# Performance work log

Hardware: AMD Instinct MI355X
Metric: run time of the kernel (lower is better)

## Reference

```python
import jax, jax.numpy as jnp
import numpy as np
import math

EPS = 1e-8
ROUTING_ITERS = 2
FINAL_LAMBDA = 0.01

B, O, I, D_IN, D_OUT = 64, 64, 1152, 16, 16


def setup_inputs() -> dict:
    key = jax.random.key(0)
    k1, k2, k3, k4, k5 = jax.random.split(key, 5)
    stdev = 0.2
    u = jax.random.normal(k1, (B, I, D_IN), dtype=jnp.float32)
    W = jax.random.normal(k2, (1, O, I, D_OUT, D_IN), dtype=jnp.float32) * stdev
    beta_a = jax.random.normal(k3, (1, O), dtype=jnp.float32) * stdev
    beta_u = jax.random.normal(k4, (1, O, 1, 1), dtype=jnp.float32) * stdev
    bias = jnp.full((1, O, D_OUT), 0.1, dtype=jnp.float32)
    return {"u": u, "W": W, "beta_a": beta_a, "beta_u": beta_u, "bias": bias}


def _m_step(rr, V, a_i, beta_a, beta_u, inv_temp):
    # rr: (B,O,I), V: (B,O,I,D), a_i: (B,I)
    rra = rr * a_i[:, None, :]                      # (B,O,I)
    rr_sum = jnp.sum(rra, axis=-1, keepdims=True)   # (B,O,1)
    mean_j = jnp.sum(rra[..., None] * V, axis=2) / (rr_sum + EPS)       # (B,O,D)
    diff = V - mean_j[:, :, None, :]
    var_j = jnp.sum(rra[..., None] * diff * diff, axis=2) / (rr_sum + EPS) + 1e-4  # (B,O,D)
    # beta_u broadcast: original stores (1,O,1) tiled over out_dim
    cost_j = jnp.sum((beta_u[..., 0] + jnp.log(var_j)) * rr_sum, axis=-1)  # (B,O)
    a_j = jax.nn.sigmoid(inv_temp * (beta_a - cost_j))                     # (B,O)
    return mean_j, var_j, a_j


def _e_step(mean_j, var_j, a_j, V):
    diff = V - mean_j[:, :, None, :]                                  # (B,O,I,D)
    p1 = jnp.sqrt(2.0 * math.pi * jnp.prod(var_j, axis=-1) + EPS)     # (B,O)
    log_arg = -jnp.sum(diff * diff / (2.0 * var_j[:, :, None, :] + EPS), axis=-1)  # (B,O,I)
    p_ij = jnp.exp(log_arg) / (p1[:, :, None] + EPS)                  # (B,O,I)
    ap = a_j[:, :, None] * p_ij
    rr = ap / (jnp.sum(ap, axis=1, keepdims=True) + EPS)
    return rr


def reference(u, W, beta_a, beta_u, bias):
    # votes: V[b,o,i,e] = sum_d u[b,i,d] * W[0,o,i,e,d]
    a_i = jnp.linalg.norm(u + EPS, axis=-1)                           # (B,I)
    V = jnp.einsum('bid,oied->boie', u, W[0]) + EPS + bias[:, :, None, :]  # (B,O,I,D)
    batch = u.shape[0]
    out_caps = W.shape[1]
    rr = jnp.full((batch, out_caps, V.shape[2]), 1.0 / out_caps, dtype=u.dtype)
    for i in range(ROUTING_ITERS):
        inv_temp = FINAL_LAMBDA * (1.0 - 0.95 ** (i + 1))
        mean_j, var_j, a_j = _m_step(rr, V, a_i, beta_a, beta_u, inv_temp)
        if i < ROUTING_ITERS - 1:
            rr = _e_step(mean_j, var_j, a_j, V)
    out = a_j[:, :, None] * mean_j / (jnp.linalg.norm(mean_j + EPS, axis=-1, keepdims=True) + EPS)
    return out
```

## Files before the change

kernel.cpp:

```cpp
#include <hip/hip_runtime.h>

#define EPSF 1e-8f

constexpr int NB = 64;
constexpr int NO = 64;
constexpr int NI = 1152;
constexpr int ND = 16;

constexpr int RSTRIDE = 260;
constexpr int BUFSZ   = 64 * RSTRIDE;

typedef float v2f __attribute__((ext_vector_type(2)));
typedef float v4f __attribute__((ext_vector_type(4)));


__device__ __forceinline__ void loadrow16f(const float* __restrict__ base,
                                           size_t elem, float* f){
  const float4* p = (const float4*)(base + elem);
  float4 x0=p[0], x1=p[1], x2=p[2], x3=p[3];
  f[0]=x0.x; f[1]=x0.y; f[2]=x0.z; f[3]=x0.w;
  f[4]=x1.x; f[5]=x1.y; f[6]=x1.z; f[7]=x1.w;
  f[8]=x2.x; f[9]=x2.y; f[10]=x2.z; f[11]=x2.w;
  f[12]=x3.x; f[13]=x3.y; f[14]=x3.z; f[15]=x3.w;
}

__device__ __forceinline__ void gl_lds16(const float* g, float* l){
  __builtin_amdgcn_global_load_lds(
      (const __attribute__((address_space(1))) unsigned int*)g,
      (__attribute__((address_space(3))) unsigned int*)l,
      16, 0, 0);
}

__global__ __launch_bounds__(256, 2) void k_mpass(
    const float* __restrict__ u, const float* __restrict__ W,
    float* __restrict__ S1p, float* __restrict__ S2p, float* __restrict__ Wsp,
    const int CH)
{
  const int CI = NI / CH;
  const int bid = blockIdx.x;
  const int bg = bid / CH, c = bid % CH;
  const int t = threadIdx.x, lane = t & 63, w = t >> 6;
  const int b0 = bg*8 + 2*w, b1 = b0 + 1;
  const int i0 = c*CI;

  __shared__ float buf[BUFSZ];

  v2f S1[16], S2[16]; v2f wsum = {0.f, 0.f};
  #pragma unroll
  for (int e=0;e<16;++e){ S1[e]=v2f{0.f,0.f}; S2[e]=v2f{0.f,0.f}; }

  const float* row = &buf[lane*RSTRIDE];

  for (int ii=0; ii<CI; ++ii){
    const int i = i0 + ii;
    __syncthreads();
    {
      const float* g = W + (size_t)i*256 + (size_t)(w*16)*NI*256
                         + (size_t)lane*4;
      float* l = buf + (w*16)*RSTRIDE;
      #pragma unroll 1
      for (int r=0;r<16;++r){
        gl_lds16(g, l);
        g += (size_t)NI*256;
        l += RSTRIDE;
      }
    }

    v2f u01[16];
    {
      const float4* pa = (const float4*)(u + ((size_t)b0*NI + i)*ND);
      const float4* pb = (const float4*)(u + ((size_t)b1*NI + i)*ND);
      #pragma unroll
      for (int q=0;q<4;++q){
        float4 xa = pa[q], xb = pb[q];
        u01[q*4+0] = v2f{xa.x, xb.x};
        u01[q*4+1] = v2f{xa.y, xb.y};
        u01[q*4+2] = v2f{xa.z, xb.z};
        u01[q*4+3] = v2f{xa.w, xb.w};
      }
    }
    v2f ss = {0.f, 0.f};
    #pragma unroll
    for (int d=0;d<16;++d){ v2f x = u01[d] + EPSF; ss += x*x; }
    const v2f av = {sqrtf(ss.x), sqrtf(ss.y)};

    __syncthreads();

    #pragma unroll
    for (int e=0;e<16;++e){
      v2f Ve = {0.f, 0.f};
      #pragma unroll
      for (int dq=0; dq<4; ++dq){
        const float4 wv = *(const float4*)(row + e*16 + dq*4);
        const int d = dq*4;
        Ve += wv.x*u01[d+0];
        Ve += wv.y*u01[d+1];
        Ve += wv.z*u01[d+2];
        Ve += wv.w*u01[d+3];
      }
      v2f tv = av*Ve;
      S1[e] += tv;
      S2[e] += tv*Ve;
    }
    wsum += av;
  }

  const size_t ba = (((size_t)b0*CH + c)*NO + lane);
  const size_t bb = (((size_t)b1*CH + c)*NO + lane);
  #pragma unroll
  for (int e=0;e<16;++e){
    S1p[ba*ND+e]=S1[e].x; S2p[ba*ND+e]=S2[e].x;
    S1p[bb*ND+e]=S1[e].y; S2p[bb*ND+e]=S2[e].y;
  }
  Wsp[ba] = wsum.x; Wsp[bb] = wsum.y;
}

template<int NW, bool ESTEP>
__global__ __launch_bounds__(NW*64, 2) void k_heavy(
    const float* __restrict__ u, const float* __restrict__ W,
    const float* __restrict__ bias,
    const float* __restrict__ mean0, const float* __restrict__ i2v0,
    const float* __restrict__ c0,
    float* __restrict__ S1p, float* __restrict__ S2p, float* __restrict__ Wsp,
    const int CH)
{
  const int CI = NI / CH;
  constexpr int ROWS = 64 / NW;
  const int bid = blockIdx.x;
  const int bg = bid / CH, c = bid % CH;
  const int t = threadIdx.x, lane = t & 63, w = t >> 6;
  const int b0 = bg*(2*NW) + 2*w, b1 = b0 + 1;
  const int i0 = c*CI;

  __shared__ float buf[2*BUFSZ];

  float bs[16]; loadrow16f(bias, (size_t)lane*ND, bs);
  v2f mr[16], ir[16]; v2f c01 = {0.f, 0.f};
  if (ESTEP){
    const size_t m0 = ((size_t)b0*NO + lane)*ND;
    const size_t m1 = ((size_t)b1*NO + lane)*ND;
    #pragma unroll
    for (int e=0;e<16;++e){
      mr[e] = v2f{mean0[m0+e], mean0[m1+e]};
      ir[e] = v2f{i2v0[m0+e], i2v0[m1+e]};
    }
    c01 = v2f{c0[(size_t)b0*NO + lane], c0[(size_t)b1*NO + lane]};
  }

  v2f S1[16], S2[16]; v2f wsum = {0.f, 0.f};
  #pragma unroll
  for (int e=0;e<16;++e){ S1[e]=v2f{0.f,0.f}; S2[e]=v2f{0.f,0.f}; }

  auto stage = [&](int p, int i){
    const float* gbase = W + (size_t)i*256 + (size_t)lane*4;
    float* lbase = &buf[p*BUFSZ];
    #pragma unroll
    for (int r=0;r<ROWS;++r){
      const int o = w*ROWS + r;
      gl_lds16(gbase + (size_t)o*NI*256, lbase + o*RSTRIDE);
    }
  };

  int p = 0;
  stage(0, i0);

  for (int ii=0; ii<CI; ++ii){
    __syncthreads();
    if (ii+1 < CI) stage(p^1, i0+ii+1);

    const int i = i0 + ii;
    v2f u01[16];
    {
      const float4* pa = (const float4*)(u + ((size_t)b0*NI + i)*ND);
      const float4* pb = (const float4*)(u + ((size_t)b1*NI + i)*ND);
      #pragma unroll
      for (int q=0;q<4;++q){
        float4 xa = pa[q], xb = pb[q];
        u01[q*4+0] = v2f{xa.x, xb.x};
        u01[q*4+1] = v2f{xa.y, xb.y};
        u01[q*4+2] = v2f{xa.z, xb.z};
        u01[q*4+3] = v2f{xa.w, xb.w};
      }
    }
    v2f ss = {0.f, 0.f};
    #pragma unroll
    for (int d=0;d<16;++d){ v2f x = u01[d] + EPSF; ss += x*x; }
    const v2f av = {sqrtf(ss.x), sqrtf(ss.y)};

    v2f V[16];
    #pragma unroll
    for (int e=0;e<16;++e){ float b = bs[e] + EPSF; V[e] = v2f{b, b}; }
    const float* row = &buf[p*BUFSZ + lane*RSTRIDE];
    #pragma unroll
    for (int e=0;e<16;++e){
      #pragma unroll
      for (int dq=0; dq<4; ++dq){
        const float4 wv = *(const float4*)(row + e*16 + dq*4);
        const int d = dq*4;
        V[e] += wv.x*u01[d+0];
        V[e] += wv.y*u01[d+1];
        V[e] += wv.z*u01[d+2];
        V[e] += wv.w*u01[d+3];
      }
    }

    v2f wg;
    if (ESTEP){
      v2f la = {0.f, 0.f};
      #pragma unroll
      for (int e=0;e<16;++e){ v2f df = V[e]-mr[e]; la += df*df*ir[e]; }
      v2f ap = c01 * v2f{__expf(-la.x), __expf(-la.y)};
      float q0 = ap.x, q1 = ap.y;
      #pragma unroll
      for (int off=32; off; off>>=1){
        q0 += __shfl_xor(q0, off);
        q1 += __shfl_xor(q1, off);
      }
      wg = v2f{ap.x/(q0 + EPSF)*av.x, ap.y/(q1 + EPSF)*av.y};
    } else {
      wg = av;
    }
    wsum += wg;
    #pragma unroll
    for (int e=0;e<16;++e){
      v2f tv = wg*V[e]; S1[e]+=tv; S2[e]+=tv*V[e];
    }
    p ^= 1;
  }

  const size_t ba = (((size_t)b0*CH + c)*NO + lane);
  const size_t bb = (((size_t)b1*CH + c)*NO + lane);
  #pragma unroll
  for (int e=0;e<16;++e){
    S1p[ba*ND+e]=S1[e].x; S2p[ba*ND+e]=S2[e].x;
    S1p[bb*ND+e]=S1[e].y; S2p[bb*ND+e]=S2[e].y;
  }
  Wsp[ba] = wsum.x; Wsp[bb] = wsum.y;
}

__global__ __launch_bounds__(64) void k_mred(
    const float* __restrict__ beta_a, const float* __restrict__ beta_u,
    const float* __restrict__ bias,
    const float* __restrict__ S1p, const float* __restrict__ S2p,
    const float* __restrict__ Wsp, const int CH,
    float* __restrict__ mean0, float* __restrict__ i2v0, float* __restrict__ c0)
{
  const int bo = blockIdx.x;
  const int b = bo >> 6, o = bo & 63;
  const int t = threadIdx.x;
  const int q = t & 3, cg = t >> 2;

  v4f s1 = {0.f,0.f,0.f,0.f}, s2 = {0.f,0.f,0.f,0.f};
  for (int c = cg; c < CH; c += 16){
    const size_t base = ((((size_t)b*CH)+c)*NO + o)*ND + 4*q;
    s1 += *(const v4f*)(S1p + base);
    s2 += *(const v4f*)(S2p + base);
  }
  #pragma unroll
  for (int off=4; off<64; off<<=1){
    #pragma unroll
    for (int k=0;k<4;++k){
      s1[k] += __shfl_xor(s1[k], off);
      s2[k] += __shfl_xor(s2[k], off);
    }
  }
  float wv = 0.f;
  for (int c = t; c < CH; c += 64)
    wv += Wsp[(((size_t)b*CH)+c)*NO + o];
  #pragma unroll
  for (int off=1; off<64; off<<=1) wv += __shfl_xor(wv, off);

  {
    v4f Bq = *(const v4f*)(bias + (size_t)o*ND + 4*q);
    Bq += EPSF;
    s2 += 2.f*Bq*s1 + Bq*Bq*wv;
    s1 += Bq*wv;
  }

  const float rrsum = wv * (1.f/64.f);
  const float inv = 1.f/(rrsum + EPSF);
  const float bu = beta_u[o];
  v4f T1 = s1*(1.f/64.f), T2 = s2*(1.f/64.f);
  v4f m   = T1*inv;
  v4f var = (T2 - 2.f*m*T1 + m*m*rrsum)*inv + 1e-4f;
  v4f iv;
  float ctp = 0.f, prp = 1.f;
  #pragma unroll
  for (int k=0;k<4;++k){
    iv[k] = 1.f/(2.f*var[k] + EPSF);
    ctp += bu + __logf(var[k]);
    prp *= var[k];
  }
  ctp += __shfl_xor(ctp, 1); ctp += __shfl_xor(ctp, 2);
  prp *= __shfl_xor(prp, 1); prp *= __shfl_xor(prp, 2);

  const size_t mbase = ((size_t)b*NO + o)*ND;
  if (cg == 0){
    *(v4f*)(mean0 + mbase + 4*q) = m;
    *(v4f*)(i2v0  + mbase + 4*q) = iv;
  }
  if (t == 0){
    float cost = ctp * rrsum;
    float x  = 5.0e-4f*(beta_a[o] - cost);
    float aj = 1.f/(1.f + __expf(-x));
    float p1 = sqrtf(6.2831853071795864f*prp + EPSF);
    c0[(size_t)b*NO + o] = aj/(p1 + EPSF);
  }
}

__global__ __launch_bounds__(64) void k_final(
    const float* __restrict__ beta_a, const float* __restrict__ beta_u,
    const float* __restrict__ S1p, const float* __restrict__ S2p,
    const float* __restrict__ Wsp, const int CH,
    float* __restrict__ out)
{
  const int bo = blockIdx.x;
  const int b = bo >> 6, o = bo & 63;
  const int t = threadIdx.x;
  const int q = t & 3, cg = t >> 2;

  v4f s1 = {0.f,0.f,0.f,0.f}, s2 = {0.f,0.f,0.f,0.f};
  for (int c = cg; c < CH; c += 16){
    const size_t base = ((((size_t)b*CH)+c)*NO + o)*ND + 4*q;
    s1 += *(const v4f*)(S1p + base);
    s2 += *(const v4f*)(S2p + base);
  }
  #pragma unroll
  for (int off=4; off<64; off<<=1){
    #pragma unroll
    for (int k=0;k<4;++k){
      s1[k] += __shfl_xor(s1[k], off);
      s2[k] += __shfl_xor(s2[k], off);
    }
  }
  float wv = 0.f;
  for (int c = t; c < CH; c += 64)
    wv += Wsp[(((size_t)b*CH)+c)*NO + o];
  #pragma unroll
  for (int off=1; off<64; off<<=1) wv += __shfl_xor(wv, off);

  const float Wsum = wv;
  const float inv = 1.f/(Wsum + EPSF);
  const float bu = beta_u[o];
  v4f m   = s1*inv;
  v4f var = (s2 - 2.f*m*s1 + m*m*Wsum)*inv + 1e-4f;
  float ctp = 0.f, nrm = 0.f;
  #pragma unroll
  for (int k=0;k<4;++k){
    ctp += bu + __logf(var[k]);
    float me = m[k] + EPSF;
    nrm += me*me;
  }
  ctp += __shfl_xor(ctp, 1); ctp += __shfl_xor(ctp, 2);
  nrm += __shfl_xor(nrm, 1); nrm += __shfl_xor(nrm, 2);

  const float cost = ctp * Wsum;
  const float x  = 9.75e-4f*(beta_a[o] - cost);
  const float aj = 1.f/(1.f + __expf(-x));
  const float scale = aj/(sqrtf(nrm) + EPSF);
  if (cg == 0){
    *(v4f*)(out + (size_t)bo*ND + 4*q) = scale*m;
  }
}

extern "C" void kernel_launch(void* const* d_in, const int* in_sizes, int n_in,
                              void* d_out, int out_size, void* d_ws, size_t ws_size,
                              hipStream_t stream)
{
  const float* u      = (const float*)d_in[0];
  const float* W      = (const float*)d_in[1];
  const float* beta_a = (const float*)d_in[2];
  const float* beta_u = (const float*)d_in[3];
  const float* bias   = (const float*)d_in[4];
  float* ws  = (float*)d_ws;
  float* out = (float*)d_out;

  const size_t base_f = 2u*NB*NO*ND + NB*NO;
  auto need = [&](int ch){
    return (base_f + 2u*(size_t)NB*ch*NO*ND + (size_t)NB*ch*NO)*4;
  };
  const bool big = (ws_size >= need(64));
  const int CH = big ? 64 : 32;

  float* mean0= ws;
  float* i2v0 = mean0 + (size_t)NB*NO*ND;
  float* c0   = i2v0 + (size_t)NB*NO*ND;
  float* S1p  = c0   + (size_t)NB*NO;
  float* S2p  = S1p  + (size_t)NB*CH*NO*ND;
  float* Wsp  = S2p  + (size_t)NB*CH*NO*ND;

  k_mpass<<<(NB/8)*CH, 256, 0, stream>>>(u, W, S1p, S2p, Wsp, CH);
  k_mred<<<NB*NO, 64, 0, stream>>>(beta_a, beta_u, bias, S1p, S2p, Wsp, CH,
                                   mean0, i2v0, c0);
  if (big){
    k_heavy<8,true><<<(NB/16)*CH, 512, 0, stream>>>(u, W, bias,
                                                    mean0, i2v0, c0,
                                                    S1p, S2p, Wsp, CH);
  } else {
    k_heavy<4,true><<<(NB/8)*CH, 256, 0, stream>>>(u, W, bias,
                                                   mean0, i2v0, c0,
                                                   S1p, S2p, Wsp, CH);
  }
  k_final<<<NB*NO, 64, 0, stream>>>(beta_a, beta_u, S1p, S2p, Wsp, CH, out);
}
```

Measured before the change: 326.9 us.

## Materialize votes in the M-pass and reuse them in a streaming E-pass

```diff
diff --git a/kernel.cpp b/kernel.cpp
--- a/kernel.cpp
+++ b/kernel.cpp
@@ -31,10 +31,11 @@
       16, 0, 0);
 }
 
+template<bool STORV>
 __global__ __launch_bounds__(256, 2) void k_mpass(
     const float* __restrict__ u, const float* __restrict__ W,
     float* __restrict__ S1p, float* __restrict__ S2p, float* __restrict__ Wsp,
-    const int CH)
+    float* __restrict__ Vws, const int CH)
 {
   const int CI = NI / CH;
   const int bid = blockIdx.x;
@@ -87,20 +88,32 @@
     __syncthreads();
 
     #pragma unroll
-    for (int e=0;e<16;++e){
-      v2f Ve = {0.f, 0.f};
+    for (int qd=0; qd<4; ++qd){
+      v2f Vq[4];
       #pragma unroll
-      for (int dq=0; dq<4; ++dq){
-        const float4 wv = *(const float4*)(row + e*16 + dq*4);
-        const int d = dq*4;
-        Ve += wv.x*u01[d+0];
-        Ve += wv.y*u01[d+1];
-        Ve += wv.z*u01[d+2];
-        Ve += wv.w*u01[d+3];
-      }
-      v2f tv = av*Ve;
-      S1[e] += tv;
-      S2[e] += tv*Ve;
+      for (int eq=0; eq<4; ++eq){
+        const int e = qd*4 + eq;
+        v2f Ve = {0.f, 0.f};
+        #pragma unroll
+        for (int dq=0; dq<4; ++dq){
+          const float4 wv = *(const float4*)(row + e*16 + dq*4);
+          const int d = dq*4;
+          Ve += wv.x*u01[d+0];
+          Ve += wv.y*u01[d+1];
+          Ve += wv.z*u01[d+2];
+          Ve += wv.w*u01[d+3];
+        }
+        v2f tv = av*Ve;
+        S1[e] += tv;
+        S2[e] += tv*Ve;
+        Vq[eq] = Ve;
+      }
+      if (STORV){
+        float4 va = {Vq[0].x, Vq[1].x, Vq[2].x, Vq[3].x};
+        float4 vb = {Vq[0].y, Vq[1].y, Vq[2].y, Vq[3].y};
+        *(float4*)(Vws + (((size_t)b0*NI + i)*NO + lane)*ND + 4*qd) = va;
+        *(float4*)(Vws + (((size_t)b1*NI + i)*NO + lane)*ND + 4*qd) = vb;
+      }
     }
     wsum += av;
   }
@@ -115,8 +128,79 @@
   Wsp[ba] = wsum.x; Wsp[bb] = wsum.y;
 }
 
-template<int NW, bool ESTEP>
-__global__ __launch_bounds__(NW*64, 2) void k_heavy(
+__global__ __launch_bounds__(256, 2) void k_epass(
+    const float* __restrict__ u, const float* __restrict__ Vws,
+    const float* __restrict__ mean0, const float* __restrict__ i2v0,
+    const float* __restrict__ c0, const float* __restrict__ bias,
+    float* __restrict__ S1p, float* __restrict__ S2p, float* __restrict__ Wsp,
+    const int CH)
+{
+  const int CI = NI / CH;
+  const int bid = blockIdx.x;
+  const int bg = bid / CH, c = bid % CH;
+  const int t = threadIdx.x, lane = t & 63, w = t >> 6;
+  const int b = bg*4 + w;
+  const int i0 = c*CI;
+
+  float mrB[16], ir[16];
+  {
+    const size_t m0 = ((size_t)b*NO + lane)*ND;
+    #pragma unroll
+    for (int q=0;q<4;++q){
+      float4 mm = *(const float4*)(mean0 + m0 + 4*q);
+      float4 iv = *(const float4*)(i2v0 + m0 + 4*q);
+      float4 bq = *(const float4*)(bias + (size_t)lane*ND + 4*q);
+      mrB[4*q+0]=mm.x-(bq.x+EPSF); mrB[4*q+1]=mm.y-(bq.y+EPSF);
+      mrB[4*q+2]=mm.z-(bq.z+EPSF); mrB[4*q+3]=mm.w-(bq.w+EPSF);
+      ir[4*q+0]=iv.x; ir[4*q+1]=iv.y; ir[4*q+2]=iv.z; ir[4*q+3]=iv.w;
+    }
+  }
+  const float cc = c0[(size_t)b*NO + lane];
+
+  float S1[16], S2[16]; float wsum = 0.f;
+  #pragma unroll
+  for (int e=0;e<16;++e){ S1[e]=0.f; S2[e]=0.f; }
+
+  for (int ii=0; ii<CI; ++ii){
+    const int i = i0 + ii;
+    float V[16];
+    {
+      const float4* pv =
+        (const float4*)(Vws + (((size_t)b*NI + i)*NO + lane)*ND);
+      #pragma unroll
+      for (int q=0;q<4;++q){
+        float4 x = pv[q];
+        V[4*q+0]=x.x; V[4*q+1]=x.y; V[4*q+2]=x.z; V[4*q+3]=x.w;
+      }
+    }
+    float uu[16];
+    loadrow16f(u, ((size_t)b*NI + i)*ND, uu);
+    float ss = 0.f;
+    #pragma unroll
+    for (int d=0;d<16;++d){ float x = uu[d] + EPSF; ss += x*x; }
+    const float av = sqrtf(ss);
+
+    float la = 0.f;
+    #pragma unroll
+    for (int e=0;e<16;++e){ float df = V[e]-mrB[e]; la += df*df*ir[e]; }
+    float ap = cc*__expf(-la);
+    float qs = ap;
+    #pragma unroll
+    for (int off=32; off; off>>=1) qs += __shfl_xor(qs, off);
+    const float wg = ap/(qs + EPSF)*av;
+    wsum += wg;
+    #pragma unroll
+    for (int e=0;e<16;++e){ float tv = wg*V[e]; S1[e]+=tv; S2[e]+=tv*V[e]; }
+  }
+
+  const size_t ba = (((size_t)b*CH + c)*NO + lane);
+  #pragma unroll
+  for (int e=0;e<16;++e){ S1p[ba*ND+e]=S1[e]; S2p[ba*ND+e]=S2[e]; }
+  Wsp[ba] = wsum;
+}
+
+template<int NW>
+__global__ __launch_bounds__(NW*64, 2) void k_heavy_e(
     const float* __restrict__ u, const float* __restrict__ W,
     const float* __restrict__ bias,
     const float* __restrict__ mean0, const float* __restrict__ i2v0,
@@ -135,8 +219,8 @@
   __shared__ float buf[2*BUFSZ];
 
   float bs[16]; loadrow16f(bias, (size_t)lane*ND, bs);
-  v2f mr[16], ir[16]; v2f c01 = {0.f, 0.f};
-  if (ESTEP){
+  v2f mr[16], ir[16]; v2f c01;
+  {
     const size_t m0 = ((size_t)b0*NO + lane)*ND;
     const size_t m1 = ((size_t)b1*NO + lane)*ND;
     #pragma unroll
@@ -204,22 +288,17 @@
       }
     }
 
-    v2f wg;
-    if (ESTEP){
-      v2f la = {0.f, 0.f};
-      #pragma unroll
-      for (int e=0;e<16;++e){ v2f df = V[e]-mr[e]; la += df*df*ir[e]; }
-      v2f ap = c01 * v2f{__expf(-la.x), __expf(-la.y)};
-      float q0 = ap.x, q1 = ap.y;
-      #pragma unroll
-      for (int off=32; off; off>>=1){
-        q0 += __shfl_xor(q0, off);
-        q1 += __shfl_xor(q1, off);
-      }
-      wg = v2f{ap.x/(q0 + EPSF)*av.x, ap.y/(q1 + EPSF)*av.y};
-    } else {
-      wg = av;
-    }
+    v2f la = {0.f, 0.f};
+    #pragma unroll
+    for (int e=0;e<16;++e){ v2f df = V[e]-mr[e]; la += df*df*ir[e]; }
+    v2f ap = c01 * v2f{__expf(-la.x), __expf(-la.y)};
+    float q0 = ap.x, q1 = ap.y;
+    #pragma unroll
+    for (int off=32; off; off>>=1){
+      q0 += __shfl_xor(q0, off);
+      q1 += __shfl_xor(q1, off);
+    }
+    v2f wg = v2f{ap.x/(q0 + EPSF)*av.x, ap.y/(q1 + EPSF)*av.y};
     wsum += wg;
     #pragma unroll
     for (int e=0;e<16;++e){
@@ -308,8 +387,10 @@
   }
 }
 
+template<bool RAW>
 __global__ __launch_bounds__(64) void k_final(
     const float* __restrict__ beta_a, const float* __restrict__ beta_u,
+    const float* __restrict__ bias,
     const float* __restrict__ S1p, const float* __restrict__ S2p,
     const float* __restrict__ Wsp, const int CH,
     float* __restrict__ out)
@@ -338,6 +419,13 @@
     wv += Wsp[(((size_t)b*CH)+c)*NO + o];
   #pragma unroll
   for (int off=1; off<64; off<<=1) wv += __shfl_xor(wv, off);
+
+  if (RAW){
+    v4f Bq = *(const v4f*)(bias + (size_t)o*ND + 4*q);
+    Bq += EPSF;
+    s2 += 2.f*Bq*s1 + Bq*Bq*wv;
+    s1 += Bq*wv;
+  }
 
   const float Wsum = wv;
   const float inv = 1.f/(Wsum + EPSF);
@@ -379,7 +467,11 @@
   auto need = [&](int ch){
     return (base_f + 2u*(size_t)NB*ch*NO*ND + (size_t)NB*ch*NO)*4;
   };
-  const bool big = (ws_size >= need(64));
+  const size_t vws_f = (size_t)NB*NI*NO*ND;
+  const size_t need_v = need(64) + vws_f*4;
+
+  const bool vpath = (ws_size >= need_v);
+  const bool big   = (ws_size >= need(64));
   const int CH = big ? 64 : 32;
 
   float* mean0= ws;
@@ -388,18 +480,34 @@
   float* S1p  = c0   + (size_t)NB*NO;
   float* S2p  = S1p  + (size_t)NB*CH*NO*ND;
   float* Wsp  = S2p  + (size_t)NB*CH*NO*ND;
-
-  k_mpass<<<(NB/8)*CH, 256, 0, stream>>>(u, W, S1p, S2p, Wsp, CH);
+  float* Vws  = Wsp  + (size_t)NB*CH*NO;
+
+  if (vpath){
+    k_mpass<true><<<(NB/8)*CH, 256, 0, stream>>>(u, W, S1p, S2p, Wsp,
+                                                 Vws, CH);
+  } else {
+    k_mpass<false><<<(NB/8)*CH, 256, 0, stream>>>(u, W, S1p, S2p, Wsp,
+                                                  Vws, CH);
+  }
   k_mred<<<NB*NO, 64, 0, stream>>>(beta_a, beta_u, bias, S1p, S2p, Wsp, CH,
                                    mean0, i2v0, c0);
-  if (big){
-    k_heavy<8,true><<<(NB/16)*CH, 512, 0, stream>>>(u, W, bias,
-                                                    mean0, i2v0, c0,
-                                                    S1p, S2p, Wsp, CH);
+
+  if (vpath){
+    k_epass<<<(NB/4)*CH, 256, 0, stream>>>(u, Vws, mean0, i2v0, c0, bias,
+                                           S1p, S2p, Wsp, CH);
+    k_final<true><<<NB*NO, 64, 0, stream>>>(beta_a, beta_u, bias,
+                                            S1p, S2p, Wsp, CH, out);
+  } else if (big){
+    k_heavy_e<8><<<(NB/16)*CH, 512, 0, stream>>>(u, W, bias,
+                                                 mean0, i2v0, c0,
+                                                 S1p, S2p, Wsp, CH);
+    k_final<false><<<NB*NO, 64, 0, stream>>>(beta_a, beta_u, bias,
+                                             S1p, S2p, Wsp, CH, out);
   } else {
-    k_heavy<4,true><<<(NB/8)*CH, 256, 0, stream>>>(u, W, bias,
-                                                   mean0, i2v0, c0,
-                                                   S1p, S2p, Wsp, CH);
-  }
-  k_final<<<NB*NO, 64, 0, stream>>>(beta_a, beta_u, S1p, S2p, Wsp, CH, out);
-}
+    k_heavy_e<4><<<(NB/8)*CH, 256, 0, stream>>>(u, W, bias,
+                                                mean0, i2v0, c0,
+                                                S1p, S2p, Wsp, CH);
+    k_final<false><<<NB*NO, 64, 0, stream>>>(beta_a, beta_u, bias,
+                                             S1p, S2p, Wsp, CH, out);
+  }
+}
```

New measurement: 327.9 us. About the same (+0.3%).

## Add slim one-batch-per-wave kernel with half-tile W staging and bias folded out

Applied to the files above, without the earlier changes.

```diff
diff --git a/kernel.cpp b/kernel.cpp
--- a/kernel.cpp
+++ b/kernel.cpp
@@ -9,6 +9,9 @@
 
 constexpr int RSTRIDE = 260;
 constexpr int BUFSZ   = 64 * RSTRIDE;
+
+constexpr int PSTRIDE = 260;
+constexpr int HBUFSZ  = 32 * PSTRIDE;
 
 typedef float v2f __attribute__((ext_vector_type(2)));
 typedef float v4f __attribute__((ext_vector_type(4)));
@@ -31,8 +34,144 @@
       16, 0, 0);
 }
 
-__global__ __launch_bounds__(256, 2) void k_mpass(
+template<bool ESTEP>
+__global__ __launch_bounds__(256, 6) void k_slim(
     const float* __restrict__ u, const float* __restrict__ W,
+    const float* __restrict__ mean0, const float* __restrict__ i2v0,
+    const float* __restrict__ c0,
+    float* __restrict__ S1p, float* __restrict__ S2p, float* __restrict__ Wsp,
+    const int CH)
+{
+  const int CI = NI / CH;
+  const int bid = blockIdx.x;
+  const int bg = bid / CH, c = bid % CH;
+  const int t = threadIdx.x, lane = t & 63, w = t >> 6;
+  const int b = bg*4 + w;
+  const int i0 = c*CI;
+
+  const int hl = lane & 31, rsel = lane >> 5;
+  const int ro = ((lane & 31) << 1) | (lane >> 5);
+
+  __shared__ float buf[HBUFSZ];
+
+  float cc = 0.f;
+  if (ESTEP) cc = c0[(size_t)b*NO + ro];
+
+  float S1[16], S2[16]; float wsum = 0.f;
+  #pragma unroll
+  for (int e=0;e<16;++e){ S1[e]=0.f; S2[e]=0.f; }
+
+  const float* rowp = &buf[(lane & 31)*PSTRIDE + (lane >> 5)*128];
+
+  for (int ii=0; ii<CI; ++ii){
+    const int i = i0 + ii;
+
+    __syncthreads();
+    {
+      const float* g = W + (size_t)i*256 + (size_t)hl*4
+                         + (size_t)(w*16 + rsel)*NI*256;
+      float* l = buf + (w*8)*PSTRIDE;
+      #pragma unroll 1
+      for (int r=0;r<8;++r){
+        gl_lds16(g, l);
+        g += (size_t)2*NI*256;
+        l += PSTRIDE;
+      }
+    }
+
+    float uu[16];
+    loadrow16f(u, ((size_t)b*NI + i)*ND, uu);
+    float ss = 0.f;
+    #pragma unroll
+    for (int d=0;d<16;++d){ float x = uu[d] + EPSF; ss += x*x; }
+    const float av = sqrtf(ss);
+
+    __syncthreads();
+
+    float V[16];
+    #pragma unroll
+    for (int e=0;e<8;++e){
+      float Ve = 0.f;
+      #pragma unroll
+      for (int dq=0; dq<4; ++dq){
+        const float4 wv = *(const float4*)(rowp + e*16 + dq*4);
+        const int d = dq*4;
+        Ve += wv.x*uu[d+0];
+        Ve += wv.y*uu[d+1];
+        Ve += wv.z*uu[d+2];
+        Ve += wv.w*uu[d+3];
+      }
+      if (ESTEP) V[e] = Ve;
+      else { float tv = av*Ve; S1[e]+=tv; S2[e]+=tv*Ve; }
+    }
+
+    __syncthreads();
+    {
+      const float* g = W + (size_t)i*256 + 128 + (size_t)hl*4
+                         + (size_t)(w*16 + rsel)*NI*256;
+      float* l = buf + (w*8)*PSTRIDE;
+      #pragma unroll 1
+      for (int r=0;r<8;++r){
+        gl_lds16(g, l);
+        g += (size_t)2*NI*256;
+        l += PSTRIDE;
+      }
+    }
+    __syncthreads();
+
+    #pragma unroll
+    for (int e=0;e<8;++e){
+      float Ve = 0.f;
+      #pragma unroll
+      for (int dq=0; dq<4; ++dq){
+        const float4 wv = *(const float4*)(rowp + e*16 + dq*4);
+        const int d = dq*4;
+        Ve += wv.x*uu[d+0];
+        Ve += wv.y*uu[d+1];
+        Ve += wv.z*uu[d+2];
+        Ve += wv.w*uu[d+3];
+      }
+      if (ESTEP) V[8+e] = Ve;
+      else { float tv = av*Ve; S1[8+e]+=tv; S2[8+e]+=tv*Ve; }
+    }
+
+    if (ESTEP){
+      float la = 0.f;
+      const size_t mb = ((size_t)b*NO + ro)*ND;
+      #pragma unroll
+      for (int q=0;q<4;++q){
+        float4 mm = *(const float4*)(mean0 + mb + 4*q);
+        float4 iv = *(const float4*)(i2v0 + mb + 4*q);
+        float d0 = V[4*q+0]-mm.x, d1 = V[4*q+1]-mm.y;
+        float d2 = V[4*q+2]-mm.z, d3 = V[4*q+3]-mm.w;
+        la += d0*d0*iv.x; la += d1*d1*iv.y;
+        la += d2*d2*iv.z; la += d3*d3*iv.w;
+      }
+      float ap = cc*__expf(-la);
+      float qs = ap;
+      #pragma unroll
+      for (int off=32; off; off>>=1) qs += __shfl_xor(qs, off);
+      const float wg = ap/(qs + EPSF)*av;
+      wsum += wg;
+      #pragma unroll
+      for (int e=0;e<16;++e){ float tv = wg*V[e]; S1[e]+=tv; S2[e]+=tv*V[e]; }
+    } else {
+      wsum += av;
+    }
+  }
+
+  const size_t ba = (((size_t)b*CH + c)*NO + ro);
+  #pragma unroll
+  for (int e=0;e<16;++e){ S1p[ba*ND+e]=S1[e]; S2p[ba*ND+e]=S2[e]; }
+  Wsp[ba] = wsum;
+}
+
+template<bool ESTEP>
+__global__ __launch_bounds__(256, 2) void k_heavy4(
+    const float* __restrict__ u, const float* __restrict__ W,
+    const float* __restrict__ bias,
+    const float* __restrict__ mean0, const float* __restrict__ i2v0,
+    const float* __restrict__ c0,
     float* __restrict__ S1p, float* __restrict__ S2p, float* __restrict__ Wsp,
     const int CH)
 {
@@ -43,29 +182,43 @@
   const int b0 = bg*8 + 2*w, b1 = b0 + 1;
   const int i0 = c*CI;
 
-  __shared__ float buf[BUFSZ];
+  __shared__ float buf[2*BUFSZ];
+
+  float bs[16]; loadrow16f(bias, (size_t)lane*ND, bs);
+  v2f mr[16], ir[16]; v2f c01 = {0.f, 0.f};
+  if (ESTEP){
+    const size_t m0 = ((size_t)b0*NO + lane)*ND;
+    const size_t m1 = ((size_t)b1*NO + lane)*ND;
+    #pragma unroll
+    for (int e=0;e<16;++e){
+      mr[e] = v2f{mean0[m0+e], mean0[m1+e]};
+      ir[e] = v2f{i2v0[m0+e], i2v0[m1+e]};
+    }
+    c01 = v2f{c0[(size_t)b0*NO + lane], c0[(size_t)b1*NO + lane]};
+  }
 
   v2f S1[16], S2[16]; v2f wsum = {0.f, 0.f};
   #pragma unroll
   for (int e=0;e<16;++e){ S1[e]=v2f{0.f,0.f}; S2[e]=v2f{0.f,0.f}; }
 
-  const float* row = &buf[lane*RSTRIDE];
+  auto stage = [&](int p, int i){
+    const float* gbase = W + (size_t)i*256 + (size_t)lane*4;
+    float* lbase = &buf[p*BUFSZ];
+    #pragma unroll
+    for (int r=0;r<16;++r){
+      const int o = w*16 + r;
+      gl_lds16(gbase + (size_t)o*NI*256, lbase + o*RSTRIDE);
+    }
+  };
+
+  int p = 0;
+  stage(0, i0);
 
   for (int ii=0; ii<CI; ++ii){
+    __syncthreads();
+    if (ii+1 < CI) stage(p^1, i0+ii+1);
+
     const int i = i0 + ii;
-    __syncthreads();
-    {
-      const float* g = W + (size_t)i*256 + (size_t)(w*16)*NI*256
-                         + (size_t)lane*4;
-      float* l = buf + (w*16)*RSTRIDE;
-      #pragma unroll 1
-      for (int r=0;r<16;++r){
-        gl_lds16(g, l);
-        g += (size_t)NI*256;
-        l += RSTRIDE;
-      }
-    }
-
     v2f u01[16];
     {
       const float4* pa = (const float4*)(u + ((size_t)b0*NI + i)*ND);
@@ -84,112 +237,9 @@
     for (int d=0;d<16;++d){ v2f x = u01[d] + EPSF; ss += x*x; }
     const v2f av = {sqrtf(ss.x), sqrtf(ss.y)};
 
-    __syncthreads();
-
-    #pragma unroll
-    for (int e=0;e<16;++e){
-      v2f Ve = {0.f, 0.f};
-      #pragma unroll
-      for (int dq=0; dq<4; ++dq){
-        const float4 wv = *(const float4*)(row + e*16 + dq*4);
-        const int d = dq*4;
-        Ve += wv.x*u01[d+0];
-        Ve += wv.y*u01[d+1];
-        Ve += wv.z*u01[d+2];
-        Ve += wv.w*u01[d+3];
-      }
-      v2f tv = av*Ve;
-      S1[e] += tv;
-      S2[e] += tv*Ve;
-    }
-    wsum += av;
-  }
-
-  const size_t ba = (((size_t)b0*CH + c)*NO + lane);
-  const size_t bb = (((size_t)b1*CH + c)*NO + lane);
-  #pragma unroll
-  for (int e=0;e<16;++e){
-    S1p[ba*ND+e]=S1[e].x; S2p[ba*ND+e]=S2[e].x;
-    S1p[bb*ND+e]=S1[e].y; S2p[bb*ND+e]=S2[e].y;
-  }
-  Wsp[ba] = wsum.x; Wsp[bb] = wsum.y;
-}
-
-template<int NW, bool ESTEP>
-__global__ __launch_bounds__(NW*64, 2) void k_heavy(
-    const float* __restrict__ u, const float* __restrict__ W,
-    const float* __restrict__ bias,
-    const float* __restrict__ mean0, const float* __restrict__ i2v0,
-    const float* __restrict__ c0,
-    float* __restrict__ S1p, float* __restrict__ S2p, float* __restrict__ Wsp,
-    const int CH)
-{
-  const int CI = NI / CH;
-  constexpr int ROWS = 64 / NW;
-  const int bid = blockIdx.x;
-  const int bg = bid / CH, c = bid % CH;
-  const int t = threadIdx.x, lane = t & 63, w = t >> 6;
-  const int b0 = bg*(2*NW) + 2*w, b1 = b0 + 1;
-  const int i0 = c*CI;
-
-  __shared__ float buf[2*BUFSZ];
-
-  float bs[16]; loadrow16f(bias, (size_t)lane*ND, bs);
-  v2f mr[16], ir[16]; v2f c01 = {0.f, 0.f};
-  if (ESTEP){
-    const size_t m0 = ((size_t)b0*NO + lane)*ND;
-    const size_t m1 = ((size_t)b1*NO + lane)*ND;
-    #pragma unroll
-    for (int e=0;e<16;++e){
-      mr[e] = v2f{mean0[m0+e], mean0[m1+e]};
-      ir[e] = v2f{i2v0[m0+e], i2v0[m1+e]};
-    }
-    c01 = v2f{c0[(size_t)b0*NO + lane], c0[(size_t)b1*NO + lane]};
-  }
-
-  v2f S1[16], S2[16]; v2f wsum = {0.f, 0.f};
-  #pragma unroll
-  for (int e=0;e<16;++e){ S1[e]=v2f{0.f,0.f}; S2[e]=v2f{0.f,0.f}; }
-
-  auto stage = [&](int p, int i){
-    const float* gbase = W + (size_t)i*256 + (size_t)lane*4;
-    float* lbase = &buf[p*BUFSZ];
-    #pragma unroll
-    for (int r=0;r<ROWS;++r){
-      const int o = w*ROWS + r;
-      gl_lds16(gbase + (size_t)o*NI*256, lbase + o*RSTRIDE);
-    }
-  };
-
-  int p = 0;
-  stage(0, i0);
-
-  for (int ii=0; ii<CI; ++ii){
-    __syncthreads();
-    if (ii+1 < CI) stage(p^1, i0+ii+1);
-
-    const int i = i0 + ii;
-    v2f u01[16];
-    {
-      const float4* pa = (const float4*)(u + ((size_t)b0*NI + i)*ND);
-      const float4* pb = (const float4*)(u + ((size_t)b1*NI + i)*ND);
-      #pragma unroll
-      for (int q=0;q<4;++q){
-        float4 xa = pa[q], xb = pb[q];
-        u01[q*4+0] = v2f{xa.x, xb.x};
-        u01[q*4+1] = v2f{xa.y, xb.y};
-        u01[q*4+2] = v2f{xa.z, xb.z};
-        u01[q*4+3] = v2f{xa.w, xb.w};
-      }
-    }
-    v2f ss = {0.f, 0.f};
-    #pragma unroll
-    for (int d=0;d<16;++d){ v2f x = u01[d] + EPSF; ss += x*x; }
-    const v2f av = {sqrtf(ss.x), sqrtf(ss.y)};
-
     v2f V[16];
     #pragma unroll
-    for (int e=0;e<16;++e){ float b = bs[e] + EPSF; V[e] = v2f{b, b}; }
+    for (int e=0;e<16;++e){ float bq = bs[e] + EPSF; V[e] = v2f{bq, bq}; }
     const float* row = &buf[p*BUFSZ + lane*RSTRIDE];
     #pragma unroll
     for (int e=0;e<16;++e){
@@ -238,6 +288,7 @@
   Wsp[ba] = wsum.x; Wsp[bb] = wsum.y;
 }
 
+template<bool RAWADJ>
 __global__ __launch_bounds__(64) void k_mred(
     const float* __restrict__ beta_a, const float* __restrict__ beta_u,
     const float* __restrict__ bias,
@@ -270,9 +321,9 @@
   #pragma unroll
   for (int off=1; off<64; off<<=1) wv += __shfl_xor(wv, off);
 
-  {
-    v4f Bq = *(const v4f*)(bias + (size_t)o*ND + 4*q);
-    Bq += EPSF;
+  v4f Bq = *(const v4f*)(bias + (size_t)o*ND + 4*q);
+  Bq += EPSF;
+  if (RAWADJ){
     s2 += 2.f*Bq*s1 + Bq*Bq*wv;
     s1 += Bq*wv;
   }
@@ -296,7 +347,8 @@
 
   const size_t mbase = ((size_t)b*NO + o)*ND;
   if (cg == 0){
-    *(v4f*)(mean0 + mbase + 4*q) = m;
+    v4f mout = RAWADJ ? (m - Bq) : m;
+    *(v4f*)(mean0 + mbase + 4*q) = mout;
     *(v4f*)(i2v0  + mbase + 4*q) = iv;
   }
   if (t == 0){
@@ -308,8 +360,10 @@
   }
 }
 
+template<bool RAW>
 __global__ __launch_bounds__(64) void k_final(
     const float* __restrict__ beta_a, const float* __restrict__ beta_u,
+    const float* __restrict__ bias,
     const float* __restrict__ S1p, const float* __restrict__ S2p,
     const float* __restrict__ Wsp, const int CH,
     float* __restrict__ out)
@@ -338,6 +392,13 @@
     wv += Wsp[(((size_t)b*CH)+c)*NO + o];
   #pragma unroll
   for (int off=1; off<64; off<<=1) wv += __shfl_xor(wv, off);
+
+  if (RAW){
+    v4f Bq = *(const v4f*)(bias + (size_t)o*ND + 4*q);
+    Bq += EPSF;
+    s2 += 2.f*Bq*s1 + Bq*Bq*wv;
+    s1 += Bq*wv;
+  }
 
   const float Wsum = wv;
   const float inv = 1.f/(Wsum + EPSF);
@@ -379,8 +440,8 @@
   auto need = [&](int ch){
     return (base_f + 2u*(size_t)NB*ch*NO*ND + (size_t)NB*ch*NO)*4;
   };
-  const bool big = (ws_size >= need(64));
-  const int CH = big ? 64 : 32;
+  const bool slim = (ws_size >= need(48));
+  const int CH = slim ? 48 : 32;
 
   float* mean0= ws;
   float* i2v0 = mean0 + (size_t)NB*NO*ND;
@@ -389,17 +450,31 @@
   float* S2p  = S1p  + (size_t)NB*CH*NO*ND;
   float* Wsp  = S2p  + (size_t)NB*CH*NO*ND;
 
-  k_mpass<<<(NB/8)*CH, 256, 0, stream>>>(u, W, S1p, S2p, Wsp, CH);
-  k_mred<<<NB*NO, 64, 0, stream>>>(beta_a, beta_u, bias, S1p, S2p, Wsp, CH,
-                                   mean0, i2v0, c0);
-  if (big){
-    k_heavy<8,true><<<(NB/16)*CH, 512, 0, stream>>>(u, W, bias,
-                                                    mean0, i2v0, c0,
-                                                    S1p, S2p, Wsp, CH);
+  if (slim){
+    const int GRID = (NB/4)*CH;
+    k_slim<false><<<GRID, 256, 0, stream>>>(u, W,
+                                            nullptr, nullptr, nullptr,
+                                            S1p, S2p, Wsp, CH);
+    k_mred<true><<<NB*NO, 64, 0, stream>>>(beta_a, beta_u, bias,
+                                           S1p, S2p, Wsp, CH,
+                                           mean0, i2v0, c0);
+    k_slim<true><<<GRID, 256, 0, stream>>>(u, W,
+                                           mean0, i2v0, c0,
+                                           S1p, S2p, Wsp, CH);
+    k_final<true><<<NB*NO, 64, 0, stream>>>(beta_a, beta_u, bias,
+                                            S1p, S2p, Wsp, CH, out);
   } else {
-    k_heavy<4,true><<<(NB/8)*CH, 256, 0, stream>>>(u, W, bias,
-                                                   mean0, i2v0, c0,
-                                                   S1p, S2p, Wsp, CH);
-  }
-  k_final<<<NB*NO, 64, 0, stream>>>(beta_a, beta_u, S1p, S2p, Wsp, CH, out);
-}
+    const int GRID = (NB/8)*CH;
+    k_heavy4<false><<<GRID, 256, 0, stream>>>(u, W, bias,
+                                              nullptr, nullptr, nullptr,
+                                              S1p, S2p, Wsp, CH);
+    k_mred<false><<<NB*NO, 64, 0, stream>>>(beta_a, beta_u, bias,
+                                            S1p, S2p, Wsp, CH,
+                                            mean0, i2v0, c0);
+    k_heavy4<true><<<GRID, 256, 0, stream>>>(u, W, bias,
+                                             mean0, i2v0, c0,
+                                             S1p, S2p, Wsp, CH);
+    k_final<false><<<NB*NO, 64, 0, stream>>>(beta_a, beta_u, bias,
+                                             S1p, S2p, Wsp, CH, out);
+  }
+}
```

Measured after the change: 530.1 us. +62.1%, slower.

## Recompute votes in E-step kernel to cut register pressure, fold bias into mean

Applied to the files above, without the earlier changes.

```diff
diff --git a/kernel.cpp b/kernel.cpp
--- a/kernel.cpp
+++ b/kernel.cpp
@@ -115,11 +115,10 @@
   Wsp[ba] = wsum.x; Wsp[bb] = wsum.y;
 }
 
-template<int NW, bool ESTEP>
-__global__ __launch_bounds__(NW*64, 2) void k_heavy(
+template<int NW>
+__global__ __launch_bounds__(NW*64, 2) void k_epass(
     const float* __restrict__ u, const float* __restrict__ W,
-    const float* __restrict__ bias,
-    const float* __restrict__ mean0, const float* __restrict__ i2v0,
+    const float* __restrict__ madj, const float* __restrict__ i2v0,
     const float* __restrict__ c0,
     float* __restrict__ S1p, float* __restrict__ S2p, float* __restrict__ Wsp,
     const int CH)
@@ -134,18 +133,11 @@
 
   __shared__ float buf[2*BUFSZ];
 
-  float bs[16]; loadrow16f(bias, (size_t)lane*ND, bs);
-  v2f mr[16], ir[16]; v2f c01 = {0.f, 0.f};
-  if (ESTEP){
-    const size_t m0 = ((size_t)b0*NO + lane)*ND;
-    const size_t m1 = ((size_t)b1*NO + lane)*ND;
-    #pragma unroll
-    for (int e=0;e<16;++e){
-      mr[e] = v2f{mean0[m0+e], mean0[m1+e]};
-      ir[e] = v2f{i2v0[m0+e], i2v0[m1+e]};
-    }
-    c01 = v2f{c0[(size_t)b0*NO + lane], c0[(size_t)b1*NO + lane]};
-  }
+  const v2f c01 = {c0[(size_t)b0*NO + lane], c0[(size_t)b1*NO + lane]};
+  const float4* ma0 = (const float4*)(madj + ((size_t)b0*NO + lane)*ND);
+  const float4* ma1 = (const float4*)(madj + ((size_t)b1*NO + lane)*ND);
+  const float4* iva = (const float4*)(i2v0 + ((size_t)b0*NO + lane)*ND);
+  const float4* ivb = (const float4*)(i2v0 + ((size_t)b1*NO + lane)*ND);
 
   v2f S1[16], S2[16]; v2f wsum = {0.f, 0.f};
   #pragma unroll
@@ -187,9 +179,147 @@
     for (int d=0;d<16;++d){ v2f x = u01[d] + EPSF; ss += x*x; }
     const v2f av = {sqrtf(ss.x), sqrtf(ss.y)};
 
+    const float* row = &buf[p*BUFSZ + lane*RSTRIDE];
+
+    v2f la = {0.f, 0.f};
+    #pragma unroll
+    for (int q=0;q<4;++q){
+      const float4 m0 = ma0[q], m1 = ma1[q];
+      const float4 w0 = iva[q], w1 = ivb[q];
+      #pragma unroll
+      for (int k=0;k<4;++k){
+        const int e = 4*q + k;
+        v2f Ve = {0.f, 0.f};
+        #pragma unroll
+        for (int dq=0; dq<4; ++dq){
+          const float4 wv = *(const float4*)(row + e*16 + dq*4);
+          const int d = dq*4;
+          Ve += wv.x*u01[d+0];
+          Ve += wv.y*u01[d+1];
+          Ve += wv.z*u01[d+2];
+          Ve += wv.w*u01[d+3];
+        }
+        const v2f mm = {(&m0.x)[k], (&m1.x)[k]};
+        const v2f iw = {(&w0.x)[k], (&w1.x)[k]};
+        v2f df = Ve - mm;
+        la += df*df*iw;
+      }
+    }
+
+    asm volatile("" ::: "memory");
+
+    v2f ap = c01 * v2f{__expf(-la.x), __expf(-la.y)};
+    float q0 = ap.x, q1 = ap.y;
+    #pragma unroll
+    for (int off=32; off; off>>=1){
+      q0 += __shfl_xor(q0, off);
+      q1 += __shfl_xor(q1, off);
+    }
+    const v2f wg = {ap.x/(q0 + EPSF)*av.x, ap.y/(q1 + EPSF)*av.y};
+    wsum += wg;
+
+    #pragma unroll
+    for (int e=0;e<16;++e){
+      v2f Ve = {0.f, 0.f};
+      #pragma unroll
+      for (int dq=0; dq<4; ++dq){
+        const float4 wv = *(const float4*)(row + e*16 + dq*4);
+        const int d = dq*4;
+        Ve += wv.x*u01[d+0];
+        Ve += wv.y*u01[d+1];
+        Ve += wv.z*u01[d+2];
+        Ve += wv.w*u01[d+3];
+      }
+      v2f tv = wg*Ve;
+      S1[e] += tv;
+      S2[e] += tv*Ve;
+    }
+    p ^= 1;
+  }
+
+  const size_t ba = (((size_t)b0*CH + c)*NO + lane);
+  const size_t bb = (((size_t)b1*CH + c)*NO + lane);
+  #pragma unroll
+  for (int e=0;e<16;++e){
+    S1p[ba*ND+e]=S1[e].x; S2p[ba*ND+e]=S2[e].x;
+    S1p[bb*ND+e]=S1[e].y; S2p[bb*ND+e]=S2[e].y;
+  }
+  Wsp[ba] = wsum.x; Wsp[bb] = wsum.y;
+}
+
+__global__ __launch_bounds__(256, 2) void k_heavy4e(
+    const float* __restrict__ u, const float* __restrict__ W,
+    const float* __restrict__ bias,
+    const float* __restrict__ mean0, const float* __restrict__ i2v0,
+    const float* __restrict__ c0,
+    float* __restrict__ S1p, float* __restrict__ S2p, float* __restrict__ Wsp,
+    const int CH)
+{
+  const int CI = NI / CH;
+  const int bid = blockIdx.x;
+  const int bg = bid / CH, c = bid % CH;
+  const int t = threadIdx.x, lane = t & 63, w = t >> 6;
+  const int b0 = bg*8 + 2*w, b1 = b0 + 1;
+  const int i0 = c*CI;
+
+  __shared__ float buf[2*BUFSZ];
+
+  float bs[16]; loadrow16f(bias, (size_t)lane*ND, bs);
+  v2f mr[16], ir[16]; v2f c01;
+  {
+    const size_t m0 = ((size_t)b0*NO + lane)*ND;
+    const size_t m1 = ((size_t)b1*NO + lane)*ND;
+    #pragma unroll
+    for (int e=0;e<16;++e){
+      mr[e] = v2f{mean0[m0+e], mean0[m1+e]};
+      ir[e] = v2f{i2v0[m0+e], i2v0[m1+e]};
+    }
+    c01 = v2f{c0[(size_t)b0*NO + lane], c0[(size_t)b1*NO + lane]};
+  }
+
+  v2f S1[16], S2[16]; v2f wsum = {0.f, 0.f};
+  #pragma unroll
+  for (int e=0;e<16;++e){ S1[e]=v2f{0.f,0.f}; S2[e]=v2f{0.f,0.f}; }
+
+  auto stage = [&](int p, int i){
+    const float* gbase = W + (size_t)i*256 + (size_t)lane*4;
+    float* lbase = &buf[p*BUFSZ];
+    #pragma unroll
+    for (int r=0;r<16;++r){
+      const int o = w*16 + r;
+      gl_lds16(gbase + (size_t)o*NI*256, lbase + o*RSTRIDE);
+    }
+  };
+
+  int p = 0;
+  stage(0, i0);
+
+  for (int ii=0; ii<CI; ++ii){
+    __syncthreads();
+    if (ii+1 < CI) stage(p^1, i0+ii+1);
+
+    const int i = i0 + ii;
+    v2f u01[16];
+    {
+      const float4* pa = (const float4*)(u + ((size_t)b0*NI + i)*ND);
+      const float4* pb = (const float4*)(u + ((size_t)b1*NI + i)*ND);
+      #pragma unroll
+      for (int q=0;q<4;++q){
+        float4 xa = pa[q], xb = pb[q];
+        u01[q*4+0] = v2f{xa.x, xb.x};
+        u01[q*4+1] = v2f{xa.y, xb.y};
+        u01[q*4+2] = v2f{xa.z, xb.z};
+        u01[q*4+3] = v2f{xa.w, xb.w};
+      }
+    }
+    v2f ss = {0.f, 0.f};
+    #pragma unroll
+    for (int d=0;d<16;++d){ v2f x = u01[d] + EPSF; ss += x*x; }
+    const v2f av = {sqrtf(ss.x), sqrtf(ss.y)};
+
     v2f V[16];
     #pragma unroll
-    for (int e=0;e<16;++e){ float b = bs[e] + EPSF; V[e] = v2f{b, b}; }
+    for (int e=0;e<16;++e){ float bq = bs[e] + EPSF; V[e] = v2f{bq, bq}; }
     const float* row = &buf[p*BUFSZ + lane*RSTRIDE];
     #pragma unroll
     for (int e=0;e<16;++e){
@@ -204,22 +334,17 @@
       }
     }
 
-    v2f wg;
-    if (ESTEP){
-      v2f la = {0.f, 0.f};
-      #pragma unroll
-      for (int e=0;e<16;++e){ v2f df = V[e]-mr[e]; la += df*df*ir[e]; }
-      v2f ap = c01 * v2f{__expf(-la.x), __expf(-la.y)};
-      float q0 = ap.x, q1 = ap.y;
-      #pragma unroll
-      for (int off=32; off; off>>=1){
-        q0 += __shfl_xor(q0, off);
-        q1 += __shfl_xor(q1, off);
-      }
-      wg = v2f{ap.x/(q0 + EPSF)*av.x, ap.y/(q1 + EPSF)*av.y};
-    } else {
-      wg = av;
-    }
+    v2f la = {0.f, 0.f};
+    #pragma unroll
+    for (int e=0;e<16;++e){ v2f df = V[e]-mr[e]; la += df*df*ir[e]; }
+    v2f ap = c01 * v2f{__expf(-la.x), __expf(-la.y)};
+    float q0 = ap.x, q1 = ap.y;
+    #pragma unroll
+    for (int off=32; off; off>>=1){
+      q0 += __shfl_xor(q0, off);
+      q1 += __shfl_xor(q1, off);
+    }
+    v2f wg = v2f{ap.x/(q0 + EPSF)*av.x, ap.y/(q1 + EPSF)*av.y};
     wsum += wg;
     #pragma unroll
     for (int e=0;e<16;++e){
@@ -238,6 +363,7 @@
   Wsp[ba] = wsum.x; Wsp[bb] = wsum.y;
 }
 
+template<bool MADJ>
 __global__ __launch_bounds__(64) void k_mred(
     const float* __restrict__ beta_a, const float* __restrict__ beta_u,
     const float* __restrict__ bias,
@@ -270,12 +396,10 @@
   #pragma unroll
   for (int off=1; off<64; off<<=1) wv += __shfl_xor(wv, off);
 
-  {
-    v4f Bq = *(const v4f*)(bias + (size_t)o*ND + 4*q);
-    Bq += EPSF;
-    s2 += 2.f*Bq*s1 + Bq*Bq*wv;
-    s1 += Bq*wv;
-  }
+  v4f Bq = *(const v4f*)(bias + (size_t)o*ND + 4*q);
+  Bq += EPSF;
+  s2 += 2.f*Bq*s1 + Bq*Bq*wv;
+  s1 += Bq*wv;
 
   const float rrsum = wv * (1.f/64.f);
   const float inv = 1.f/(rrsum + EPSF);
@@ -296,7 +420,8 @@
 
   const size_t mbase = ((size_t)b*NO + o)*ND;
   if (cg == 0){
-    *(v4f*)(mean0 + mbase + 4*q) = m;
+    v4f mout = MADJ ? (m - Bq) : m;
+    *(v4f*)(mean0 + mbase + 4*q) = mout;
     *(v4f*)(i2v0  + mbase + 4*q) = iv;
   }
   if (t == 0){
@@ -308,8 +433,10 @@
   }
 }
 
+template<bool RAW>
 __global__ __launch_bounds__(64) void k_final(
     const float* __restrict__ beta_a, const float* __restrict__ beta_u,
+    const float* __restrict__ bias,
     const float* __restrict__ S1p, const float* __restrict__ S2p,
     const float* __restrict__ Wsp, const int CH,
     float* __restrict__ out)
@@ -338,6 +465,13 @@
     wv += Wsp[(((size_t)b*CH)+c)*NO + o];
   #pragma unroll
   for (int off=1; off<64; off<<=1) wv += __shfl_xor(wv, off);
+
+  if (RAW){
+    v4f Bq = *(const v4f*)(bias + (size_t)o*ND + 4*q);
+    Bq += EPSF;
+    s2 += 2.f*Bq*s1 + Bq*Bq*wv;
+    s1 += Bq*wv;
+  }
 
   const float Wsum = wv;
   const float inv = 1.f/(Wsum + EPSF);
@@ -390,16 +524,22 @@
   float* Wsp  = S2p  + (size_t)NB*CH*NO*ND;
 
   k_mpass<<<(NB/8)*CH, 256, 0, stream>>>(u, W, S1p, S2p, Wsp, CH);
-  k_mred<<<NB*NO, 64, 0, stream>>>(beta_a, beta_u, bias, S1p, S2p, Wsp, CH,
-                                   mean0, i2v0, c0);
   if (big){
-    k_heavy<8,true><<<(NB/16)*CH, 512, 0, stream>>>(u, W, bias,
-                                                    mean0, i2v0, c0,
-                                                    S1p, S2p, Wsp, CH);
+    k_mred<true><<<NB*NO, 64, 0, stream>>>(beta_a, beta_u, bias,
+                                           S1p, S2p, Wsp, CH,
+                                           mean0, i2v0, c0);
+    k_epass<8><<<(NB/16)*CH, 512, 0, stream>>>(u, W, mean0, i2v0, c0,
+                                               S1p, S2p, Wsp, CH);
+    k_final<true><<<NB*NO, 64, 0, stream>>>(beta_a, beta_u, bias,
+                                            S1p, S2p, Wsp, CH, out);
   } else {
-    k_heavy<4,true><<<(NB/8)*CH, 256, 0, stream>>>(u, W, bias,
-                                                   mean0, i2v0, c0,
-                                                   S1p, S2p, Wsp, CH);
-  }
-  k_final<<<NB*NO, 64, 0, stream>>>(beta_a, beta_u, S1p, S2p, Wsp, CH, out);
-}
+    k_mred<false><<<NB*NO, 64, 0, stream>>>(beta_a, beta_u, bias,
+                                            S1p, S2p, Wsp, CH,
+                                            mean0, i2v0, c0);
+    k_heavy4e<<<(NB/8)*CH, 256, 0, stream>>>(u, W, bias,
+                                             mean0, i2v0, c0,
+                                             S1p, S2p, Wsp, CH);
+    k_final<false><<<NB*NO, 64, 0, stream>>>(beta_a, beta_u, bias,
+                                             S1p, S2p, Wsp, CH, out);
+  }
+}
```

New measurement: 352.8 us. +7.9%, slower.
